# Optimization experiments

Hardware: AMD Instinct MI355X
Metric: run time of the kernel (lower is better)

Reference implementation:

```python
import jax, jax.numpy as jnp
import numpy as np

D_MODEL = 1024
N_HEADS = 16
HEAD_DIM = D_MODEL // N_HEADS
FF_DIM = 1024  # repo bug: linear2 is Linear(d_model, ff_dim); ff_dim==d_model required for residual
EPS = 1e-5


def _linear_params(k, d_in, d_out):
    kw, kb = jax.random.split(k)
    bound = 1.0 / np.sqrt(d_in)
    W = jax.random.uniform(kw, (d_out, d_in), minval=-bound, maxval=bound, dtype=jnp.float32)
    b = jax.random.uniform(kb, (d_out,), minval=-bound, maxval=bound, dtype=jnp.float32)
    return W, b


def setup_inputs() -> dict:
    key = jax.random.key(0)
    ks = jax.random.split(key, 8)
    src = jax.random.normal(ks[0], (4, 2048, D_MODEL), dtype=jnp.float32)
    Wq, bq = _linear_params(ks[1], D_MODEL, D_MODEL)
    Wk, bk = _linear_params(ks[2], D_MODEL, D_MODEL)
    Wv, bv = _linear_params(ks[3], D_MODEL, D_MODEL)
    Wo, bo = _linear_params(ks[4], D_MODEL, D_MODEL)
    W1, b1 = _linear_params(ks[5], D_MODEL, FF_DIM)
    W2, b2 = _linear_params(ks[6], D_MODEL, FF_DIM)
    g1 = jnp.ones((D_MODEL,), jnp.float32); be1 = jnp.zeros((D_MODEL,), jnp.float32)
    g2 = jnp.ones((D_MODEL,), jnp.float32); be2 = jnp.zeros((D_MODEL,), jnp.float32)
    return {"src": src, "Wq": Wq, "bq": bq, "Wk": Wk, "bk": bk, "Wv": Wv, "bv": bv,
            "Wo": Wo, "bo": bo, "W1": W1, "b1": b1, "W2": W2, "b2": b2,
            "g1": g1, "be1": be1, "g2": g2, "be2": be2}


def _layernorm(x, g, b):
    mu = jnp.mean(x, axis=-1, keepdims=True)
    var = jnp.var(x, axis=-1, keepdims=True)
    return (x - mu) * jax.lax.rsqrt(var + EPS) * g + b


def _mha(x, Wq, bq, Wk, bk, Wv, bv, Wo, bo):
    B, S, _ = x.shape
    def proj(W, b):
        return (x @ W.T + b).reshape(B, S, N_HEADS, HEAD_DIM).transpose(0, 2, 1, 3)
    Q, K, V = proj(Wq, bq), proj(Wk, bk), proj(Wv, bv)
    scale = jnp.float32(np.sqrt(HEAD_DIM))
    energy = jnp.einsum('bhqd,bhkd->bhqk', Q, K) / scale
    attn = jax.nn.softmax(energy, axis=-1)
    out = jnp.einsum('bhqk,bhkd->bhqd', attn, V)
    out = out.transpose(0, 2, 1, 3).reshape(B, S, D_MODEL)
    return out @ Wo.T + bo


def reference(src, Wq, bq, Wk, bk, Wv, bv, Wo, bo, W1, b1, W2, b2, g1, be1, g2, be2):
    x = src
    x = x + _mha(_layernorm(x, g1, be1), Wq, bq, Wk, bk, Wv, bv, Wo, bo)
    h = _layernorm(x, g2, be2)
    ff = jax.nn.relu(h @ W1.T + b1) @ W2.T + b2
    return x + ff
```

## Files before the change

### kernel.cpp

```cpp
#include <hip/hip_runtime.h>
#include <stdint.h>

typedef __attribute__((ext_vector_type(8))) short    bf16x8;
typedef __attribute__((ext_vector_type(4))) short    bf16x4;
typedef __attribute__((ext_vector_type(4))) float    f32x4;
typedef __attribute__((ext_vector_type(8))) uint16_t u16x8;
typedef __attribute__((ext_vector_type(4))) uint16_t u16x4;

#define D_MODEL 1024
#define SEQ     2048
#define NB      4
#define NH      16
#define HD      64
#define MTOK    8192

__device__ __forceinline__ float bf2f(uint16_t u) {
    union { uint32_t i; float f; } x; x.i = ((uint32_t)u) << 16; return x.f;
}
__device__ __forceinline__ uint16_t f2bf(float f) {
    union { float f; uint32_t i; } x; x.f = f;
    uint32_t r = (x.i + 0x7fffu + ((x.i >> 16) & 1u)) >> 16;
    return (uint16_t)r;
}
__device__ __forceinline__ void gload16(const void* g, void* l) {
    __builtin_amdgcn_global_load_lds(
        (const __attribute__((address_space(1))) unsigned int*)g,
        (__attribute__((address_space(3))) unsigned int*)l, 16, 0, 0);
}
__device__ __forceinline__ bf16x8 lds_ld8(const uint16_t* p) {
    bf16x4 a = *(const bf16x4*)p;
    bf16x4 b = *(const bf16x4*)(p + 4);
    bf16x8 r;
    r[0] = a[0]; r[1] = a[1]; r[2] = a[2]; r[3] = a[3];
    r[4] = b[0]; r[5] = b[1]; r[6] = b[2]; r[7] = b[3];
    return r;
}
__device__ __forceinline__ uint32_t pk_bf16_trunc(float lo, float hi) {
    return __builtin_amdgcn_perm(__float_as_uint(hi), __float_as_uint(lo), 0x07060302u);
}

__global__ __launch_bounds__(256)
void cvt_all(const float* __restrict__ s0, const float* __restrict__ s1,
             const float* __restrict__ s2, const float* __restrict__ s3,
             const float* __restrict__ s4, const float* __restrict__ s5,
             uint16_t* __restrict__ dQKV, uint16_t* __restrict__ dWo,
             uint16_t* __restrict__ dW1, uint16_t* __restrict__ dW2)
{
    const float* srcs[6] = {s0, s1, s2, s3, s4, s5};
    uint16_t* dsts[6] = {dQKV, dQKV + (size_t)D_MODEL * D_MODEL,
                         dQKV + 2 * (size_t)D_MODEL * D_MODEL, dWo, dW1, dW2};
    const float* in = srcs[blockIdx.y];
    uint16_t* out = dsts[blockIdx.y];
    const int i = (blockIdx.x * 256 + threadIdx.x) * 4;
    float4 v = *(const float4*)(in + i);
    u16x4 o;
    o[0] = f2bf(v.x); o[1] = f2bf(v.y); o[2] = f2bf(v.z); o[3] = f2bf(v.w);
    *(u16x4*)(out + i) = o;
}

__global__ __launch_bounds__(256)
void ln_kernel(const float* __restrict__ x, const float* __restrict__ g,
               const float* __restrict__ be, uint16_t* __restrict__ y)
{
    const int row = blockIdx.x;
    const int tid = threadIdx.x;
    const size_t base = (size_t)row * D_MODEL + tid * 4;
    float4 v = *(const float4*)(x + base);
    float f[4] = {v.x, v.y, v.z, v.w};
    float sum = 0.f, sq = 0.f;
#pragma unroll
    for (int e = 0; e < 4; e++) { sum += f[e]; sq += f[e] * f[e]; }
#pragma unroll
    for (int o = 32; o > 0; o >>= 1) { sum += __shfl_down(sum, o); sq += __shfl_down(sq, o); }
    __shared__ float ps[4], pq[4];
    const int lane = tid & 63, wid = tid >> 6;
    if (lane == 0) { ps[wid] = sum; pq[wid] = sq; }
    __syncthreads();
    const float ts = ps[0] + ps[1] + ps[2] + ps[3];
    const float tq = pq[0] + pq[1] + pq[2] + pq[3];
    const float mean = ts * (1.0f / D_MODEL);
    const float var  = tq * (1.0f / D_MODEL) - mean * mean;
    const float rstd = rsqrtf(var + 1e-5f);
    float4 gv = *(const float4*)(g + tid * 4);
    float4 bv = *(const float4*)(be + tid * 4);
    const float gg[4] = {gv.x, gv.y, gv.z, gv.w};
    const float bb[4] = {bv.x, bv.y, bv.z, bv.w};
    u16x4 outv;
#pragma unroll
    for (int e = 0; e < 4; e++)
        outv[e] = f2bf((f[e] - mean) * rstd * gg[e] + bb[e]);
    *(u16x4*)(y + base) = outv;
}

template<int RESID, int RELU, int OUTF32>
__global__ __launch_bounds__(256, 4)
void gemm_bt64(const uint16_t* __restrict__ A, const uint16_t* __restrict__ W,
               const float* __restrict__ bias, const float* __restrict__ resid,
               void* __restrict__ Cv)
{
    __shared__ uint16_t lA[64 * 32];
    __shared__ uint16_t lB[128 * 32];
    const int tid  = threadIdx.x;
    const int lane = tid & 63;
    const int quad = lane >> 4;
    const int l16  = lane & 15;
    const int wid  = tid >> 6;
    const int wm   = wid >> 1;
    const int wn   = wid & 1;
    const int m0   = blockIdx.y * 64;
    const int n0   = blockIdx.x * 128;

    f32x4 acc[2][4];
#pragma unroll
    for (int i = 0; i < 2; i++)
#pragma unroll
        for (int j = 0; j < 4; j++) acc[i][j] = (f32x4){0.f, 0.f, 0.f, 0.f};

    const int sr = tid >> 2;
    const int sc = (tid & 3) * 8;
    const uint16_t* gA0 = A + (size_t)(m0 + sr) * D_MODEL + sc;
    const uint16_t* gW0 = W + (size_t)(n0 + sr) * D_MODEL + sc;
    const uint16_t* gW1 = gW0 + (size_t)64 * D_MODEL;
    uint16_t* sA0 = &lA[tid * 8];
    uint16_t* sB0 = &lB[tid * 8];
    uint16_t* sB1 = sB0 + 2048;

    for (int k0 = 0; k0 < D_MODEL; k0 += 32) {
        __syncthreads();
        gload16(gA0 + k0, sA0);
        gload16(gW0 + k0, sB0);
        gload16(gW1 + k0, sB1);
        __syncthreads();
        bf16x8 af[2], bfr[4];
#pragma unroll
        for (int i = 0; i < 2; i++)
            af[i] = *(const bf16x8*)&lA[(wm * 32 + i * 16 + l16) * 32 + quad * 8];
#pragma unroll
        for (int j = 0; j < 4; j++)
            bfr[j] = *(const bf16x8*)&lB[(wn * 64 + j * 16 + l16) * 32 + quad * 8];
#pragma unroll
        for (int i = 0; i < 2; i++)
#pragma unroll
            for (int j = 0; j < 4; j++)
                acc[i][j] = __builtin_amdgcn_mfma_f32_16x16x32_bf16(af[i], bfr[j], acc[i][j], 0, 0, 0);
    }

#pragma unroll
    for (int j = 0; j < 4; j++) {
        const int col = n0 + wn * 64 + j * 16 + l16;
        const float bv = bias[col];
#pragma unroll
        for (int i = 0; i < 2; i++) {
            const int row = m0 + wm * 32 + i * 16 + quad * 4;
#pragma unroll
            for (int r = 0; r < 4; r++) {
                float v = acc[i][j][r] + bv;
                const size_t idx = (size_t)(row + r) * D_MODEL + col;
                if (RESID) v += resid[idx];
                if (RELU)  v = fmaxf(v, 0.0f);
                if (OUTF32) ((float*)Cv)[idx] = v;
                else        ((uint16_t*)Cv)[idx] = f2bf(v);
            }
        }
    }
}

#define QSCALE 0.18033688f
__global__ __launch_bounds__(256, 3)
void gemm_qkv(const uint16_t* __restrict__ A, const uint16_t* __restrict__ Wqkv,
              const float* __restrict__ bq, const float* __restrict__ bk,
              const float* __restrict__ bv, uint16_t* __restrict__ Qb,
              uint16_t* __restrict__ Kb, uint16_t* __restrict__ Vt)
{
    __shared__ uint16_t lA[128 * 32];
    __shared__ uint16_t lB[128 * 32];
    const int tid  = threadIdx.x;
    const int lane = tid & 63;
    const int quad = lane >> 4;
    const int l16  = lane & 15;
    const int wid  = tid >> 6;
    const int wm   = wid >> 1;
    const int wn   = wid & 1;
    const int t0   = blockIdx.y * 128;
    const int n0   = blockIdx.x * 128;
    const int which = n0 >> 10;
    const int lc0   = n0 & 1023;

    f32x4 acc[4][4];
#pragma unroll
    for (int i = 0; i < 4; i++)
#pragma unroll
        for (int j = 0; j < 4; j++) acc[i][j] = (f32x4){0.f, 0.f, 0.f, 0.f};

    const int sr = tid >> 2;
    const int sc = (tid & 3) * 8;
    const uint16_t* gA0 = A + (size_t)(t0 + sr) * D_MODEL + sc;
    const uint16_t* gA1 = gA0 + (size_t)64 * D_MODEL;
    const uint16_t* gW0 = Wqkv + (size_t)(n0 + sr) * D_MODEL + sc;
    const uint16_t* gW1 = gW0 + (size_t)64 * D_MODEL;
    uint16_t* sA0 = &lA[tid * 8];
    uint16_t* sA1 = sA0 + 2048;
    uint16_t* sB0 = &lB[tid * 8];
    uint16_t* sB1 = sB0 + 2048;

    for (int k0 = 0; k0 < D_MODEL; k0 += 32) {
        __syncthreads();
        gload16(gA0 + k0, sA0);
        gload16(gA1 + k0, sA1);
        gload16(gW0 + k0, sB0);
        gload16(gW1 + k0, sB1);
        __syncthreads();
        bf16x8 fa[4], fb[4];
        if (which != 2) {
#pragma unroll
            for (int i = 0; i < 4; i++)
                fa[i] = *(const bf16x8*)&lA[(wm * 64 + i * 16 + l16) * 32 + quad * 8];
#pragma unroll
            for (int j = 0; j < 4; j++)
                fb[j] = *(const bf16x8*)&lB[(wn * 64 + j * 16 + l16) * 32 + quad * 8];
        } else {
#pragma unroll
            for (int i = 0; i < 4; i++)
                fa[i] = *(const bf16x8*)&lB[(wm * 64 + i * 16 + l16) * 32 + quad * 8];
#pragma unroll
            for (int j = 0; j < 4; j++)
                fb[j] = *(const bf16x8*)&lA[(wn * 64 + j * 16 + l16) * 32 + quad * 8];
        }
#pragma unroll
        for (int i = 0; i < 4; i++)
#pragma unroll
            for (int j = 0; j < 4; j++)
                acc[i][j] = __builtin_amdgcn_mfma_f32_16x16x32_bf16(fa[i], fb[j], acc[i][j], 0, 0, 0);
    }

    if (which != 2) {
        const float* bias = (which == 0) ? bq : bk;
        uint16_t* C = (which == 0) ? Qb : Kb;
        const float alpha = (which == 0) ? QSCALE : 1.0f;
#pragma unroll
        for (int j = 0; j < 4; j++) {
            const int col = lc0 + wn * 64 + j * 16 + l16;
            const float bvv = bias[col];
#pragma unroll
            for (int i = 0; i < 4; i++) {
                const int row = t0 + wm * 64 + i * 16 + quad * 4;
#pragma unroll
                for (int r = 0; r < 4; r++)
                    C[(size_t)(row + r) * D_MODEL + col] = f2bf((acc[i][j][r] + bvv) * alpha);
            }
        }
    } else {
#pragma unroll
        for (int i = 0; i < 4; i++) {
#pragma unroll
            for (int r = 0; r < 4; r++) {
                const int wrow = lc0 + wm * 64 + i * 16 + quad * 4 + r;
                const float bvv = bv[wrow];
#pragma unroll
                for (int j = 0; j < 4; j++) {
                    const int tok = t0 + wn * 64 + j * 16 + l16;
                    Vt[(size_t)wrow * MTOK + tok] = f2bf(acc[i][j][r] + bvv);
                }
            }
        }
    }
}

#define PST 68
__global__ __launch_bounds__(256, 4)
void attn_kernel(const uint16_t* __restrict__ Q, const uint16_t* __restrict__ K,
                 const uint16_t* __restrict__ Vt, uint16_t* __restrict__ O)
{
    __shared__ uint16_t sQP[128 * PST];
    __shared__ uint16_t sK [64 * PST];
    __shared__ uint16_t sVt[64 * PST];
    __shared__ float    sSt[128];

    const int tid  = threadIdx.x;
    const int lane = tid & 63;
    const int quad = lane >> 4;
    const int l16  = lane & 15;
    const int w    = tid >> 6;

    const int q0 = blockIdx.x * 128;
    const int h  = blockIdx.y;
    const int b  = blockIdx.z;
    const size_t headoff = (size_t)h * HD;
    const size_t bbase   = (size_t)b * SEQ;

    const int r8 = tid >> 3;
    const int c8 = (tid & 7) * 8;

#pragma unroll
    for (int i = 0; i < 4; i++)
        gload16(Q + (bbase + q0 + i * 32 + r8) * D_MODEL + headoff + c8, &sQP[i * 2048 + tid * 8]);
    __syncthreads();

    bf16x8 qa[2][2];
#pragma unroll
    for (int i = 0; i < 2; i++)
#pragma unroll
        for (int ks = 0; ks < 2; ks++)
            qa[i][ks] = *(const bf16x8*)&sQP[(w * 32 + i * 16 + l16) * 64 + ks * 32 + quad * 8];

    f32x4 oacc[2][4];
#pragma unroll
    for (int i = 0; i < 2; i++)
#pragma unroll
        for (int n = 0; n < 4; n++) oacc[i][n] = (f32x4){0.f, 0.f, 0.f, 0.f};
    float mrun[2] = {-3.0e38f, -3.0e38f};
    float lrun[2] = {0.f, 0.f};

    const uint16_t* gK  = K  + bbase * D_MODEL + headoff;
    const uint16_t* gVt = Vt + headoff * MTOK + bbase;

    for (int kv0 = 0; kv0 < SEQ; kv0 += 64) {
        u16x8 kreg[2], vreg[2];
#pragma unroll
        for (int i = 0; i < 2; i++) {
            const int row = i * 32 + r8;
            kreg[i] = *(const u16x8*)(gK + (size_t)(kv0 + row) * D_MODEL + c8);
            vreg[i] = *(const u16x8*)(gVt + (size_t)row * MTOK + kv0 + c8);
        }
        __syncthreads();
#pragma unroll
        for (int i = 0; i < 2; i++) {
            const int row = i * 32 + r8;
            *(u16x4*)&sK [(size_t)row * PST + c8]     = (u16x4){kreg[i][0], kreg[i][1], kreg[i][2], kreg[i][3]};
            *(u16x4*)&sK [(size_t)row * PST + c8 + 4] = (u16x4){kreg[i][4], kreg[i][5], kreg[i][6], kreg[i][7]};
            *(u16x4*)&sVt[(size_t)row * PST + c8]     = (u16x4){vreg[i][0], vreg[i][1], vreg[i][2], vreg[i][3]};
            *(u16x4*)&sVt[(size_t)row * PST + c8 + 4] = (u16x4){vreg[i][4], vreg[i][5], vreg[i][6], vreg[i][7]};
        }
        __syncthreads();

        f32x4 st[4][2];
#pragma unroll
        for (int j = 0; j < 4; j++)
#pragma unroll
            for (int i = 0; i < 2; i++) st[j][i] = (f32x4){0.f, 0.f, 0.f, 0.f};
#pragma unroll
        for (int ks = 0; ks < 2; ks++)
#pragma unroll
            for (int j = 0; j < 4; j++) {
                bf16x8 kb = lds_ld8(&sK[(j * 16 + l16) * PST + ks * 32 + quad * 8]);
#pragma unroll
                for (int i = 0; i < 2; i++)
                    st[j][i] = __builtin_amdgcn_mfma_f32_16x16x32_bf16(kb, qa[i][ks], st[j][i], 0, 0, 0);
            }

#pragma unroll
        for (int i = 0; i < 2; i++) {
            float mx = -3.0e38f;
#pragma unroll
            for (int j = 0; j < 4; j++)
#pragma unroll
                for (int r = 0; r < 4; r++) mx = fmaxf(mx, st[j][i][r]);
            mx = fmaxf(mx, __shfl_xor(mx, 16));
            mx = fmaxf(mx, __shfl_xor(mx, 32));
            const float mnew = fmaxf(mrun[i], mx);
            const float al   = __builtin_amdgcn_exp2f(mrun[i] - mnew);
            float rs = 0.f;
#pragma unroll
            for (int j = 0; j < 4; j++)
#pragma unroll
                for (int r = 0; r < 4; r++) {
                    const float p = __builtin_amdgcn_exp2f(st[j][i][r] - mnew);
                    st[j][i][r] = p;
                    rs += p;
                }
            rs += __shfl_xor(rs, 16);
            rs += __shfl_xor(rs, 32);
            lrun[i] = lrun[i] * al + rs;
            mrun[i] = mnew;
            sSt[w * 32 + i * 16 + l16] = al;
#pragma unroll
            for (int j = 0; j < 4; j++) {
                uint2 pk;
                pk.x = pk_bf16_trunc(st[j][i][0], st[j][i][1]);
                pk.y = pk_bf16_trunc(st[j][i][2], st[j][i][3]);
                *(uint2*)&sQP[(size_t)(w * 32 + i * 16 + l16) * PST + j * 16 + quad * 4] = pk;
            }
        }

#pragma unroll
        for (int i = 0; i < 2; i++)
#pragma unroll
            for (int r = 0; r < 4; r++) {
                const float al = sSt[w * 32 + i * 16 + quad * 4 + r];
#pragma unroll
                for (int n = 0; n < 4; n++) oacc[i][n][r] *= al;
            }

#pragma unroll
        for (int i = 0; i < 2; i++)
#pragma unroll
            for (int ks = 0; ks < 2; ks++) {
                bf16x8 pa = lds_ld8(&sQP[(size_t)(w * 32 + i * 16 + l16) * PST + ks * 32 + quad * 8]);
#pragma unroll
                for (int n = 0; n < 4; n++) {
                    bf16x8 vb = lds_ld8(&sVt[(n * 16 + l16) * PST + ks * 32 + quad * 8]);
                    oacc[i][n] = __builtin_amdgcn_mfma_f32_16x16x32_bf16(pa, vb, oacc[i][n], 0, 0, 0);
                }
            }
    }

#pragma unroll
    for (int i = 0; i < 2; i++)
        sSt[w * 32 + i * 16 + l16] = 1.0f / lrun[i];
#pragma unroll
    for (int i = 0; i < 2; i++)
#pragma unroll
        for (int r = 0; r < 4; r++) {
            const size_t row = bbase + q0 + w * 32 + i * 16 + quad * 4 + r;
            const float inv = sSt[w * 32 + i * 16 + quad * 4 + r];
#pragma unroll
            for (int n = 0; n < 4; n++)
                O[row * D_MODEL + headoff + n * 16 + l16] = f2bf(oacc[i][n][r] * inv);
        }
}

extern "C" void kernel_launch(void* const* d_in, const int* in_sizes, int n_in,
                              void* d_out, int out_size, void* d_ws, size_t ws_size,
                              hipStream_t stream)
{
    const float* src = (const float*)d_in[0];
    const float* Wq  = (const float*)d_in[1];
    const float* bq  = (const float*)d_in[2];
    const float* Wk  = (const float*)d_in[3];
    const float* bk  = (const float*)d_in[4];
    const float* Wv  = (const float*)d_in[5];
    const float* bv  = (const float*)d_in[6];
    const float* Wo  = (const float*)d_in[7];
    const float* bo  = (const float*)d_in[8];
    const float* W1  = (const float*)d_in[9];
    const float* b1  = (const float*)d_in[10];
    const float* W2  = (const float*)d_in[11];
    const float* b2  = (const float*)d_in[12];
    const float* g1  = (const float*)d_in[13];
    const float* be1 = (const float*)d_in[14];
    const float* g2  = (const float*)d_in[15];
    const float* be2 = (const float*)d_in[16];
    float* out = (float*)d_out;

    uint16_t* ws  = (uint16_t*)d_ws;
    const size_t BUF = (size_t)MTOK * D_MODEL;
    const size_t WSZ = (size_t)D_MODEL * D_MODEL;
    uint16_t* xn1  = ws;
    uint16_t* Vtb  = ws + BUF;
    uint16_t* wQKV = ws + 2 * BUF;
    uint16_t* wWo  = wQKV + 3 * WSZ;
    uint16_t* wW1  = wWo + WSZ;
    uint16_t* wW2  = wW1 + WSZ;
    uint16_t* Qb   = (uint16_t*)d_out;
    uint16_t* Kb   = Qb + BUF;
    float*    x2   = (float*)d_out;

    dim3 blk(256);
    cvt_all<<<dim3(1024, 6), 256, 0, stream>>>(Wq, Wk, Wv, Wo, W1, W2, wQKV, wWo, wW1, wW2);
    ln_kernel<<<8192, 256, 0, stream>>>(src, g1, be1, xn1);
    gemm_qkv<<<dim3(24, 64), blk, 0, stream>>>(xn1, wQKV, bq, bk, bv, Qb, Kb, Vtb);
    attn_kernel<<<dim3(16, NH, NB), 256, 0, stream>>>(Qb, Kb, Vtb, xn1);
    gemm_bt64<1, 0, 1><<<dim3(8, 128), blk, 0, stream>>>(xn1, wWo, bo, src, x2);
    ln_kernel<<<8192, 256, 0, stream>>>(x2, g2, be2, xn1);
    gemm_bt64<0, 1, 0><<<dim3(8, 128), blk, 0, stream>>>(xn1, wW1, b1, nullptr, Vtb);
    gemm_bt64<1, 0, 1><<<dim3(8, 128), blk, 0, stream>>>(Vtb, wW2, b2, x2, out);
}
```

Measured before the change: 409.5 us.

## Register-prefetch next K-tile in GEMM and attention loops to overlap loads

Replaces the direct global-to-LDS loads in the two GEMM kernels and the attention KV loop with a register-staged software pipeline. The next tile is loaded into registers while MFMAs run on the current LDS tile, then written to LDS at the start of the next iteration. The aim is to hide global memory latency that was previously exposed between the two barriers. It costs extra VGPRs per thread, which may reduce occupancy.

```diff
diff --git a/kernel.cpp b/kernel.cpp
--- a/kernel.cpp
+++ b/kernel.cpp
@@ -125,12 +125,21 @@
     uint16_t* sB0 = &lB[tid * 8];
     uint16_t* sB1 = sB0 + 2048;
 
+    u16x8 ra  = *(const u16x8*)(gA0);
+    u16x8 rw0 = *(const u16x8*)(gW0);
+    u16x8 rw1 = *(const u16x8*)(gW1);
+
     for (int k0 = 0; k0 < D_MODEL; k0 += 32) {
         __syncthreads();
-        gload16(gA0 + k0, sA0);
-        gload16(gW0 + k0, sB0);
-        gload16(gW1 + k0, sB1);
-        __syncthreads();
+        *(u16x8*)sA0 = ra;
+        *(u16x8*)sB0 = rw0;
+        *(u16x8*)sB1 = rw1;
+        __syncthreads();
+        if (k0 + 32 < D_MODEL) {
+            ra  = *(const u16x8*)(gA0 + k0 + 32);
+            rw0 = *(const u16x8*)(gW0 + k0 + 32);
+            rw1 = *(const u16x8*)(gW1 + k0 + 32);
+        }
         bf16x8 af[2], bfr[4];
 #pragma unroll
         for (int i = 0; i < 2; i++)
@@ -203,13 +212,24 @@
     uint16_t* sB0 = &lB[tid * 8];
     uint16_t* sB1 = sB0 + 2048;
 
+    u16x8 ra0 = *(const u16x8*)(gA0);
+    u16x8 ra1 = *(const u16x8*)(gA1);
+    u16x8 rw0 = *(const u16x8*)(gW0);
+    u16x8 rw1 = *(const u16x8*)(gW1);
+
     for (int k0 = 0; k0 < D_MODEL; k0 += 32) {
         __syncthreads();
-        gload16(gA0 + k0, sA0);
-        gload16(gA1 + k0, sA1);
-        gload16(gW0 + k0, sB0);
-        gload16(gW1 + k0, sB1);
-        __syncthreads();
+        *(u16x8*)sA0 = ra0;
+        *(u16x8*)sA1 = ra1;
+        *(u16x8*)sB0 = rw0;
+        *(u16x8*)sB1 = rw1;
+        __syncthreads();
+        if (k0 + 32 < D_MODEL) {
+            ra0 = *(const u16x8*)(gA0 + k0 + 32);
+            ra1 = *(const u16x8*)(gA1 + k0 + 32);
+            rw0 = *(const u16x8*)(gW0 + k0 + 32);
+            rw1 = *(const u16x8*)(gW1 + k0 + 32);
+        }
         bf16x8 fa[4], fb[4];
         if (which != 2) {
 #pragma unroll
@@ -314,14 +334,15 @@
     const uint16_t* gK  = K  + bbase * D_MODEL + headoff;
     const uint16_t* gVt = Vt + headoff * MTOK + bbase;
 
+    u16x8 kreg[2], vreg[2];
+#pragma unroll
+    for (int i = 0; i < 2; i++) {
+        const int row = i * 32 + r8;
+        kreg[i] = *(const u16x8*)(gK + (size_t)row * D_MODEL + c8);
+        vreg[i] = *(const u16x8*)(gVt + (size_t)row * MTOK + c8);
+    }
+
     for (int kv0 = 0; kv0 < SEQ; kv0 += 64) {
-        u16x8 kreg[2], vreg[2];
-#pragma unroll
-        for (int i = 0; i < 2; i++) {
-            const int row = i * 32 + r8;
-            kreg[i] = *(const u16x8*)(gK + (size_t)(kv0 + row) * D_MODEL + c8);
-            vreg[i] = *(const u16x8*)(gVt + (size_t)row * MTOK + kv0 + c8);
-        }
         __syncthreads();
 #pragma unroll
         for (int i = 0; i < 2; i++) {
@@ -332,6 +353,14 @@
             *(u16x4*)&sVt[(size_t)row * PST + c8 + 4] = (u16x4){vreg[i][4], vreg[i][5], vreg[i][6], vreg[i][7]};
         }
         __syncthreads();
+        if (kv0 + 64 < SEQ) {
+#pragma unroll
+            for (int i = 0; i < 2; i++) {
+                const int row = i * 32 + r8;
+                kreg[i] = *(const u16x8*)(gK + (size_t)(kv0 + 64 + row) * D_MODEL + c8);
+                vreg[i] = *(const u16x8*)(gVt + (size_t)row * MTOK + kv0 + 64 + c8);
+            }
+        }
 
         f32x4 st[4][2];
 #pragma unroll
```

Result: slower. 449.2 us (+9.7%).
